# Performance work log

Measured on AMD Instinct MI355X. Metric: run time of the kernel, lower is better.

## Reference

```python
import jax, jax.numpy as jnp
import numpy as np

N, E, F_NODE, F_EDGE, HID, B, GDIM, ACT = 50000, 1600000, 32, 8, 256, 64, 16, 64
N_HIDDEN_LAYERS = 3


def setup_inputs() -> dict:
    key = jax.random.key(0)
    ks = jax.random.split(key, 16)
    x = jax.random.normal(ks[0], (N, F_NODE), jnp.float32)
    edge_index = jax.random.randint(ks[1], (2, E), 0, N, jnp.int64)
    edge_attr = jax.random.normal(ks[2], (E, F_EDGE), jnp.float32)
    batch = jnp.sort(jax.random.randint(ks[3], (N,), 0, B, jnp.int64))
    global_feats = jax.random.normal(ks[4], (B, GDIM), jnp.float32)
    s = lambda *d: 1.0 / np.sqrt(d[-2])
    # layer 0: node_feat -> hidden ; layers 1..3: hidden -> hidden
    We0 = jax.random.normal(ks[5], (F_EDGE, F_NODE), jnp.float32) * (1.0 / np.sqrt(F_EDGE))
    W0 = jax.random.normal(ks[6], (F_NODE, HID), jnp.float32) * (1.0 / np.sqrt(F_NODE))
    b0 = jnp.zeros((HID,), jnp.float32)
    We = jax.random.normal(ks[7], (N_HIDDEN_LAYERS, F_EDGE, HID), jnp.float32) * (1.0 / np.sqrt(F_EDGE))
    W = jax.random.normal(ks[8], (N_HIDDEN_LAYERS, HID, HID), jnp.float32) * (1.0 / np.sqrt(HID))
    b = jnp.zeros((N_HIDDEN_LAYERS, HID), jnp.float32)
    Wp = jax.random.normal(ks[9], (HID + GDIM, ACT), jnp.float32) * (1.0 / np.sqrt(HID + GDIM))
    bp = jnp.zeros((ACT,), jnp.float32)
    Wv = jax.random.normal(ks[10], (HID + GDIM, 1), jnp.float32) * (1.0 / np.sqrt(HID + GDIM))
    bv = jnp.zeros((1,), jnp.float32)
    return {"x": x, "edge_attr": edge_attr, "global_feats": global_feats,
            "We0": We0, "W0": W0, "b0": b0, "We": We, "W": W, "b": b,
            "Wp": Wp, "bp": bp, "Wv": Wv, "bv": bv,
            "edge_index": edge_index, "batch": batch}


def reference(x, edge_attr, global_feats, We0, W0, b0, We, W, b, Wp, bp, Wv, bv, edge_index, batch):
    src, dst = edge_index[0], edge_index[1]
    n_nodes = x.shape[0]
    n_graphs = global_feats.shape[0]

    def conv(h, We_l, W_l, b_l):
        # GINE-style: message relu(x_j + proj(e_ij)), sum-aggregate, node update MLP
        m = jax.nn.relu(h[src] + edge_attr @ We_l)            # [E, d]
        agg = jax.ops.segment_sum(m, dst, num_segments=n_nodes)
        return jax.nn.relu((h + agg) @ W_l + b_l)             # [N, hidden]

    h = conv(x, We0, W0, b0)
    for i in range(We.shape[0]):
        h = conv(h, We[i], W[i], b[i])

    counts = jax.ops.segment_sum(jnp.ones((n_nodes, 1), h.dtype), batch, num_segments=n_graphs)
    pooled = jax.ops.segment_sum(h, batch, num_segments=n_graphs) / jnp.maximum(counts, 1.0)
    feats = jnp.concatenate([pooled, global_feats], axis=-1)  # [B, hidden+gdim]
    logits = feats @ Wp + bp                                  # [B, max_action_dim]
    value = feats @ Wv + bv                                   # [B, 1]
    return logits, value
```

## Files before the change

kernel.cpp:

```cpp
#include <hip/hip_runtime.h>
#include <hip/hip_bf16.h>

#define NNODES 50000
#define NEDGES 1600000
#define FNODE 32
#define FEDGE 8
#define HIDD 256
#define NGRAPH 64
#define GDIM 16
#define NACT 64
#define FEATD (HIDD + GDIM)
#define PCH 8

typedef short bf16x8 __attribute__((ext_vector_type(8)));
typedef float f32x4 __attribute__((ext_vector_type(4)));
typedef __bf16 bf16x2 __attribute__((ext_vector_type(2)));


__device__ inline float bfl(uint u) {
  union { uint i; float f; } v; v.i = u << 16; return v.f;
}
__device__ inline float bfh(uint u) {
  union { uint i; float f; } v; v.i = u & 0xffff0000u; return v.f;
}
__device__ inline float bf1(ushort u) {
  union { uint i; float f; } v; v.i = ((uint)u) << 16; return v.f;
}
__device__ inline ushort f2b(float a) {
  __hip_bfloat16 h = __float2bfloat16(a);
  return *(ushort*)&h;
}
__device__ inline uint packbf(float a, float b) {
  return (uint)f2b(a) | ((uint)f2b(b) << 16);
}

__device__ inline float dot2bf(uint a, uint b, float c) {
#if defined(__has_builtin)
#if __has_builtin(__builtin_amdgcn_fdot2_f32_bf16)
  union { uint u; bf16x2 v; } ua, ub;
  ua.u = a; ub.u = b;
  return __builtin_amdgcn_fdot2_f32_bf16(ua.v, ub.v, c, false);
#else
  return fmaf(bfl(a), bfl(b), fmaf(bfh(a), bfh(b), c));
#endif
#else
  return fmaf(bfl(a), bfl(b), fmaf(bfh(a), bfh(b), c));
#endif
}


__global__ void k_zero_i32(int* __restrict__ p, int n) {
  int i = blockIdx.x * blockDim.x + threadIdx.x;
  if (i < n) p[i] = 0;
}

__global__ void k_scan1(int* __restrict__ data, int n, int* __restrict__ sums) {
  __shared__ int buf[1024];
  int gid = blockIdx.x * 1024 + threadIdx.x;
  int v = (gid < n) ? data[gid] : 0;
  buf[threadIdx.x] = v;
  __syncthreads();
  for (int d = 1; d < 1024; d <<= 1) {
    int t = (threadIdx.x >= d) ? buf[threadIdx.x - d] : 0;
    __syncthreads();
    buf[threadIdx.x] += t;
    __syncthreads();
  }
  if (gid < n) data[gid] = buf[threadIdx.x];
  if (threadIdx.x == 1023) sums[blockIdx.x] = buf[1023];
}

__global__ void k_scan3(int* __restrict__ data, int n, const int* __restrict__ sums,
                        int* __restrict__ cur) {
  int base = 0;
  for (int i = 0; i < (int)blockIdx.x; ++i) base += sums[i];
  int gid = blockIdx.x * 1024 + threadIdx.x;
  if (gid < n) {
    int v = data[gid] + base;
    data[gid] = v;
    if (gid < NNODES) cur[gid] = v;
  }
}

__global__ void k_scatter(const int* __restrict__ src, const int* __restrict__ dst,
                          int* __restrict__ cur, const float* __restrict__ ea,
                          int* __restrict__ csr_src, ushort* __restrict__ eab) {
  int e = blockIdx.x * blockDim.x + threadIdx.x;
  if (e >= NEDGES) return;
  int d = dst[e];
  int pos = atomicAdd(&cur[d], 1);
  csr_src[pos] = src[e] * 64;
  float4 a = *(const float4*)&ea[(size_t)e * FEDGE];
  float4 b = *(const float4*)&ea[(size_t)e * FEDGE + 4];
  uint4 o;
  o.x = packbf(a.x, a.y);
  o.y = packbf(a.z, a.w);
  o.z = packbf(b.x, b.y);
  o.w = packbf(b.z, b.w);
  *(uint4*)&eab[(size_t)pos * FEDGE] = o;
}


#define CVT_N (NNODES * FNODE / 4)
#define WEP_N (128 + 3 * 1024)
#define WP_N (1024 + 3 * 8192)

__global__ void k_hist_prep(const int* __restrict__ dst, int* __restrict__ off,
                            const float* __restrict__ x, ushort* __restrict__ xb,
                            const float* __restrict__ We0, const float* __restrict__ We,
                            uint* __restrict__ wep0, uint* __restrict__ wep,
                            const float* __restrict__ W0, const float* __restrict__ W,
                            ushort* __restrict__ wp0, ushort* __restrict__ wp) {
  int gid = blockIdx.x * blockDim.x + threadIdx.x;
  if (gid < NEDGES) atomicAdd(&off[dst[gid] + 1], 1);
  int i = gid;
  if (i < CVT_N) {
    float4 v = *(const float4*)&x[(size_t)i * 4];
    uint2 o;
    o.x = packbf(v.x, v.y);
    o.y = packbf(v.z, v.w);
    *(uint2*)&xb[(size_t)i * 4] = o;
    return;
  }
  i -= CVT_N;
  if (i < WEP_N) {
    if (i < 128) {
      int k2 = i >> 5, c = i & 31;
      wep0[i] = packbf(We0[(2 * k2) * FNODE + c], We0[(2 * k2 + 1) * FNODE + c]);
    } else {
      int u = i - 128;
      int l = u >> 10;
      int r = u & 1023;
      int k2 = r >> 8, c = r & 255;
      const float* Wl = We + (size_t)l * FEDGE * HIDD;
      wep[u] = packbf(Wl[(2 * k2) * HIDD + c], Wl[(2 * k2 + 1) * HIDD + c]);
    }
    return;
  }
  i -= WEP_N;
  if (i < WP_N) {
    if (i < 1024) {
      int lane = i & 63;
      int nf = i >> 6;
      int col = nf * 16 + (lane & 15);
      int k0 = (lane >> 4) * 8;
      ushort o[8];
#pragma unroll
      for (int q = 0; q < 8; ++q) o[q] = f2b(W0[(size_t)(k0 + q) * HIDD + col]);
      *(uint4*)&wp0[(size_t)i * 8] = *(uint4*)o;
    } else {
      int u = i - 1024;
      int l = u / 8192;
      int r = u - l * 8192;
      int lane = r & 63;
      int frag = r >> 6;
      int nf = frag & 15, ks = frag >> 4;
      int col = nf * 16 + (lane & 15);
      int k0 = ks * 32 + (lane >> 4) * 8;
      const float* Wl = W + (size_t)l * HIDD * HIDD;
      ushort o[8];
#pragma unroll
      for (int q = 0; q < 8; ++q) o[q] = f2b(Wl[(size_t)(k0 + q) * HIDD + col]);
      *(uint4*)&wp[(size_t)u * 8] = *(uint4*)o;
    }
  }
}


__global__ __launch_bounds__(256) void k_edge32(
    const float* __restrict__ x, const ushort* __restrict__ xb,
    const uint4* __restrict__ eab4, const uint* __restrict__ wep0,
    const int* __restrict__ off, const int* __restrict__ csr_src,
    ushort* __restrict__ t0b) {
  int wid = __builtin_amdgcn_readfirstlane(
      (int)((blockIdx.x * blockDim.x + threadIdx.x) >> 6));
  if (wid >= NNODES) return;
  int lane = threadIdx.x & 63;
  int j = lane >> 5;
  int c = lane & 31;
  uint c2 = (uint)c * 2;
  const char* xbase = (const char*)xb;
  uint w0 = wep0[c], w1 = wep0[32 + c], w2 = wep0[64 + c], w3 = wep0[96 + c];
  int s0 = off[wid], s1 = off[wid + 1];
  float acc = 0.f;
  int e = s0 + j;
  for (; e + 6 < s1; e += 8) {
    ushort hA = *(const ushort*)(xbase + ((uint)csr_src[e] + c2));
    ushort hB = *(const ushort*)(xbase + ((uint)csr_src[e + 2] + c2));
    ushort hC = *(const ushort*)(xbase + ((uint)csr_src[e + 4] + c2));
    ushort hD = *(const ushort*)(xbase + ((uint)csr_src[e + 6] + c2));
    uint4 eA = eab4[e];
    uint4 eB = eab4[e + 2];
    uint4 eC = eab4[e + 4];
    uint4 eD = eab4[e + 6];
    float pr;
#define B32(hu, eu)                 \
    pr = bf1(hu);                   \
    pr = dot2bf(eu.x, w0, pr);      \
    pr = dot2bf(eu.y, w1, pr);      \
    pr = dot2bf(eu.z, w2, pr);      \
    pr = dot2bf(eu.w, w3, pr);      \
    acc += fmaxf(pr, 0.f);
    B32(hA, eA) B32(hB, eB) B32(hC, eC) B32(hD, eD)
  }
  for (; e < s1; e += 2) {
    ushort hu = *(const ushort*)(xbase + ((uint)csr_src[e] + c2));
    uint4 eu = eab4[e];
    float pr;
    B32(hu, eu)
#undef B32
  }
  acc += __shfl_xor(acc, 32);
  if (j == 0) t0b[wid * FNODE + c] = f2b(x[wid * FNODE + c] + acc);
}


__device__ inline void body_dot(uint2 hu, uint4 eu, const uint4 wq[4], float4& acc) {
  float4 pr;
  pr.x = bfl(hu.x);
  pr.y = bfh(hu.x);
  pr.z = bfl(hu.y);
  pr.w = bfh(hu.y);
  pr.x = dot2bf(eu.x, wq[0].x, pr.x);
  pr.x = dot2bf(eu.y, wq[1].x, pr.x);
  pr.x = dot2bf(eu.z, wq[2].x, pr.x);
  pr.x = dot2bf(eu.w, wq[3].x, pr.x);
  pr.y = dot2bf(eu.x, wq[0].y, pr.y);
  pr.y = dot2bf(eu.y, wq[1].y, pr.y);
  pr.y = dot2bf(eu.z, wq[2].y, pr.y);
  pr.y = dot2bf(eu.w, wq[3].y, pr.y);
  pr.z = dot2bf(eu.x, wq[0].z, pr.z);
  pr.z = dot2bf(eu.y, wq[1].z, pr.z);
  pr.z = dot2bf(eu.z, wq[2].z, pr.z);
  pr.z = dot2bf(eu.w, wq[3].z, pr.z);
  pr.w = dot2bf(eu.x, wq[0].w, pr.w);
  pr.w = dot2bf(eu.y, wq[1].w, pr.w);
  pr.w = dot2bf(eu.z, wq[2].w, pr.w);
  pr.w = dot2bf(eu.w, wq[3].w, pr.w);
  acc.x += fmaxf(pr.x, 0.f);
  acc.y += fmaxf(pr.y, 0.f);
  acc.z += fmaxf(pr.z, 0.f);
  acc.w += fmaxf(pr.w, 0.f);
}

#define LOADCH(H, E_, eb)                                                   \
  _Pragma("unroll") for (int u = 0; u < 4; ++u) {                           \
    uint boff = ((uint)csr_src[(eb) + u] << 3) + c8;                        \
    H[u] = *(const uint2*)(hbase + boff);                                   \
  }                                                                         \
  _Pragma("unroll") for (int u = 0; u < 4; ++u) E_[u] = eab4[(eb) + u];

#define COMPCH(H, E_)                                                       \
  _Pragma("unroll") for (int u = 0; u < 4; ++u)                             \
    body_dot(H[u], E_[u], wq, (u & 1) ? acc1 : acc0);

__global__ __launch_bounds__(256) void k_edge256(
    const ushort* __restrict__ hb, const uint4* __restrict__ eab4,
    const uint* __restrict__ wepl, const int* __restrict__ off,
    const int* __restrict__ csr_src, ushort* __restrict__ tb) {
  int wid = __builtin_amdgcn_readfirstlane(
      (int)((blockIdx.x * blockDim.x + threadIdx.x) >> 6));
  if (wid >= NNODES) return;
  int lane = threadIdx.x & 63;
  int c = lane * 4;
  uint c8 = (uint)lane * 8;
  const char* hbase = (const char*)hb;
  uint4 wq[4];
#pragma unroll
  for (int k2 = 0; k2 < 4; ++k2) wq[k2] = *(const uint4*)&wepl[k2 * HIDD + c];
  int s0 = off[wid], s1 = off[wid + 1];
  float4 acc0 = {0.f, 0.f, 0.f, 0.f}, acc1 = {0.f, 0.f, 0.f, 0.f};
  int e = s0;
  int nch = (s1 - s0) >> 2;
  if (nch > 0) {
    uint2 hA[4], hB[4];
    uint4 EA[4], EB[4];
    LOADCH(hA, EA, e)
    int t = 1;
    for (; t + 1 < nch; t += 2) {
      LOADCH(hB, EB, e + 4)
      COMPCH(hA, EA)
      LOADCH(hA, EA, e + 8)
      COMPCH(hB, EB)
      e += 8;
    }
    if (t < nch) {
      LOADCH(hB, EB, e + 4)
      COMPCH(hA, EA)
      COMPCH(hB, EB)
      e += 8;
    } else {
      COMPCH(hA, EA)
      e += 4;
    }
  }
  for (; e < s1; ++e) {
    uint boff = ((uint)csr_src[e] << 3) + c8;
    uint2 hu = *(const uint2*)(hbase + boff);
    uint4 eu = eab4[e];
    body_dot(hu, eu, wq, acc0);
  }

  uint2 su = *(const uint2*)&hb[(size_t)wid * HIDD + c];
  float4 o;
  o.x = bfl(su.x) + acc0.x + acc1.x;
  o.y = bfh(su.x) + acc0.y + acc1.y;
  o.z = bfl(su.y) + acc0.z + acc1.z;
  o.w = bfh(su.y) + acc0.w + acc1.w;
  uint2 ob;
  ob.x = packbf(o.x, o.y);
  ob.y = packbf(o.z, o.w);
  *(uint2*)&tb[(size_t)wid * HIDD + c] = ob;
}
#undef LOADCH
#undef COMPCH


template <int K>
__global__ __launch_bounds__(256) void k_gemm_mfma(
    const ushort* __restrict__ Tb, const ushort* __restrict__ Wp,
    const float* __restrict__ bias, ushort* __restrict__ outb, int nrows) {
  constexpr int KS = K / 32;
  constexpr int KSH = (KS >= 2) ? 2 : KS;
  constexpr int CH = KSH * 16 * 64;
  __shared__ ushort bl[CH * 8];
  const int tid = threadIdx.x;
  const int wave = tid >> 6;
  const int lane = tid & 63;
  const int row0 = blockIdx.x * 64 + wave * 16;
  const int arow = row0 + (lane & 15);
  const int kgrp = lane >> 4;
  f32x4 acc[16];
#pragma unroll
  for (int nf = 0; nf < 16; ++nf) acc[nf] = (f32x4){0.f, 0.f, 0.f, 0.f};
#pragma unroll
  for (int st = 0; st < KS / KSH; ++st) {
    __syncthreads();
#pragma unroll
    for (int chk = 0; chk < CH / 256; ++chk) {
      int ch = chk * 256 + tid;
      *(uint4*)&bl[(size_t)ch * 8] = *(const uint4*)&Wp[((size_t)st * CH + ch) * 8];
    }
    __syncthreads();
#pragma unroll
    for (int ksl = 0; ksl < KSH; ++ksl) {
      int ks = st * KSH + ksl;
      bf16x8 af = *(const bf16x8*)&Tb[(size_t)arow * K + ks * 32 + kgrp * 8];
#pragma unroll
      for (int nf = 0; nf < 16; ++nf) {
        bf16x8 bfg = *(const bf16x8*)&bl[((size_t)(ksl * 16 + nf) * 64 + lane) * 8];
        acc[nf] = __builtin_amdgcn_mfma_f32_16x16x32_bf16(af, bfg, acc[nf], 0, 0, 0);
      }
    }
  }
  const int ocol0 = lane & 15;
  const int orow0 = row0 + (lane >> 4) * 4;
#pragma unroll
  for (int nf = 0; nf < 16; ++nf) {
    int col = nf * 16 + ocol0;
    float bv = bias[col];
#pragma unroll
    for (int r = 0; r < 4; ++r) {
      int row = orow0 + r;
      if (row < nrows) outb[(size_t)row * HIDD + col] = f2b(fmaxf(acc[nf][r] + bv, 0.f));
    }
  }
}


__global__ void k_pool_partial(const ushort* __restrict__ hb, const int* __restrict__ batch,
                               float* __restrict__ fp) {
  int b = blockIdx.x >> 3;
  int j = blockIdx.x & 7;
  __shared__ int srange[2];
  if (threadIdx.x < 2) {
    int target = b + threadIdx.x;
    int lo = 0, hi = NNODES;
    while (lo < hi) {
      int mid = (lo + hi) >> 1;
      if (batch[mid] < target) lo = mid + 1; else hi = mid;
    }
    srange[threadIdx.x] = lo;
  }
  __syncthreads();
  int s = srange[0], eend = srange[1];
  int len = eend - s;
  int cs = s + (int)((long long)len * j / PCH);
  int ce = s + (int)((long long)len * (j + 1) / PCH);
  int col = threadIdx.x;
  float acc = 0.f;
  for (int n = cs; n < ce; ++n) acc += bf1(hb[(size_t)n * HIDD + col]);
  fp[((size_t)j * NGRAPH + b) * HIDD + col] = acc;
}


__global__ void k_pool_heads(const float* __restrict__ fp, const int* __restrict__ batch,
                             const float* __restrict__ gf, const float* __restrict__ Wp,
                             const float* __restrict__ bp, const float* __restrict__ Wv,
                             const float* __restrict__ bv, float* __restrict__ out) {
  int b = blockIdx.x;
  __shared__ float f[FEATD];
  __shared__ int srange[2];
  if (threadIdx.x < 2) {
    int target = b + threadIdx.x;
    int lo = 0, hi = NNODES;
    while (lo < hi) {
      int mid = (lo + hi) >> 1;
      if (batch[mid] < target) lo = mid + 1; else hi = mid;
    }
    srange[threadIdx.x] = lo;
  }
  __syncthreads();
  int col = threadIdx.x;
  float acc = 0.f;
#pragma unroll
  for (int j = 0; j < PCH; ++j) acc += fp[((size_t)j * NGRAPH + b) * HIDD + col];
  float cnt = fmaxf((float)(srange[1] - srange[0]), 1.0f);
  f[col] = acc / cnt;
  if (col < GDIM) f[HIDD + col] = gf[b * GDIM + col];
  __syncthreads();
  if (col < NACT) {
    float lg = bp[col];
    for (int k = 0; k < FEATD; ++k) lg = fmaf(f[k], Wp[k * NACT + col], lg);
    out[b * NACT + col] = lg;
  } else if (col < 128) {
    int t = col - 64;
    float pv = 0.f;
    for (int k = t; k < FEATD; k += 64) pv = fmaf(f[k], Wv[k], pv);
#pragma unroll
    for (int d = 32; d > 0; d >>= 1) pv += __shfl_down(pv, d);
    if (t == 0) out[NGRAPH * NACT + b] = pv + bv[0];
  }
}


extern "C" void kernel_launch(void* const* d_in, const int* in_sizes, int n_in,
                              void* d_out, int out_size, void* d_ws, size_t ws_size,
                              hipStream_t stream) {
  const float* x   = (const float*)d_in[0];
  const float* ea  = (const float*)d_in[1];
  const float* gf  = (const float*)d_in[2];
  const float* We0 = (const float*)d_in[3];
  const float* W0  = (const float*)d_in[4];
  const float* b0  = (const float*)d_in[5];
  const float* We  = (const float*)d_in[6];
  const float* W   = (const float*)d_in[7];
  const float* bb  = (const float*)d_in[8];
  const float* Wp  = (const float*)d_in[9];
  const float* bp  = (const float*)d_in[10];
  const float* Wv  = (const float*)d_in[11];
  const float* bv  = (const float*)d_in[12];
  const int* eidx  = (const int*)d_in[13];
  const int* batch = (const int*)d_in[14];
  const int* esrc = eidx;
  const int* edst = eidx + NEDGES;

  char* w = (char*)d_ws;
  size_t p = 0;
  auto take = [&](size_t bytes) {
    size_t r = p;
    p += (bytes + 255) & ~(size_t)255;
    return r;
  };
  int* off      = (int*)(w + take((NNODES + 1) * 4));
  int* cur      = (int*)(w + take(NNODES * 4));
  int* sums     = (int*)(w + take(1024));
  int* csr_src  = (int*)(w + take((size_t)NEDGES * 4));
  ushort* eab   = (ushort*)(w + take((size_t)NEDGES * FEDGE * 2));
  ushort* t0b   = (ushort*)(w + take((size_t)NNODES * FNODE * 2));
  ushort* xb    = (ushort*)(w + take((size_t)NNODES * FNODE * 2));
  ushort* tb    = (ushort*)(w + take((size_t)NNODES * HIDD * 2));
  ushort* hb    = (ushort*)(w + take((size_t)NNODES * HIDD * 2));
  uint* wep0    = (uint*)(w + take(128 * 4));
  uint* wepb    = (uint*)(w + take(3 * 1024 * 4));
  ushort* wp0   = (ushort*)(w + take((size_t)1024 * 8 * 2));
  ushort* wpb   = (ushort*)(w + take((size_t)3 * 8192 * 8 * 2));
  float* fp     = (float*)(w + take((size_t)PCH * NGRAPH * HIDD * 4));
  if (p > ws_size) return;

  k_zero_i32<<<(NNODES + 1 + 255) / 256, 256, 0, stream>>>(off, NNODES + 1);
  k_hist_prep<<<(NEDGES + 255) / 256, 256, 0, stream>>>(
      edst, off, x, xb, We0, We, wep0, wepb, W0, W, wp0, wpb);
  int n_scan = NNODES + 1;
  int nb_scan = (n_scan + 1023) / 1024;
  k_scan1<<<nb_scan, 1024, 0, stream>>>(off, n_scan, sums);
  k_scan3<<<nb_scan, 1024, 0, stream>>>(off, n_scan, sums, cur);
  k_scatter<<<(NEDGES + 255) / 256, 256, 0, stream>>>(esrc, edst, cur, ea, csr_src, eab);

  const int gemm_grid = (NNODES + 63) / 64;

  k_edge32<<<NNODES / 4, 256, 0, stream>>>(x, xb, (const uint4*)eab, wep0, off,
                                           csr_src, t0b);
  k_gemm_mfma<FNODE><<<gemm_grid, 256, 0, stream>>>(t0b, wp0, b0, hb, NNODES);

  for (int l = 0; l < 3; ++l) {
    k_edge256<<<NNODES / 4, 256, 0, stream>>>(hb, (const uint4*)eab, wepb + l * 1024,
                                              off, csr_src, tb);
    k_gemm_mfma<HIDD><<<gemm_grid, 256, 0, stream>>>(
        tb, wpb + (size_t)l * 8192 * 8, bb + (size_t)l * HIDD, hb, NNODES);
  }

  k_pool_partial<<<NGRAPH * PCH, HIDD, 0, stream>>>(hb, batch, fp);
  k_pool_heads<<<NGRAPH, HIDD, 0, stream>>>(fp, batch, gf, Wp, bp, Wv, bv,
                                            (float*)d_out);
}
```

Baseline: 692.7 us.

## Split CSR scatter into permutation pass and gather-reorder; use fp32 FMA edge projection

The CSR build now scatters only edge ids through the atomic cursor, then a second kernel gathers src and edge attributes in destination order, so the writes to csr_src and eab become coalesced instead of random. This adds a kernel launch and an extra 1.6M-entry index array, and the gathers of src and edge_attr become random reads in exchange. Separately, the hidden-layer edge kernel unpacks the bf16 edge-projection weights to fp32 registers once and replaces the dot2 bf16 instructions with plain fp32 FMAs, which adds register pressure and per-edge unpack work for the edge features.

Measured after the change: 807.4 us. +16.6%, slower.

```diff
diff --git a/kernel.cpp b/kernel.cpp
--- a/kernel.cpp
+++ b/kernel.cpp
@@ -82,13 +82,20 @@
   }
 }
 
-__global__ void k_scatter(const int* __restrict__ src, const int* __restrict__ dst,
-                          int* __restrict__ cur, const float* __restrict__ ea,
-                          int* __restrict__ csr_src, ushort* __restrict__ eab) {
+__global__ void k_scatter_lite(const int* __restrict__ dst, int* __restrict__ cur,
+                               int* __restrict__ peid) {
   int e = blockIdx.x * blockDim.x + threadIdx.x;
   if (e >= NEDGES) return;
-  int d = dst[e];
-  int pos = atomicAdd(&cur[d], 1);
+  int pos = atomicAdd(&cur[dst[e]], 1);
+  peid[pos] = e;
+}
+
+__global__ void k_reorder(const int* __restrict__ peid, const int* __restrict__ src,
+                          const float* __restrict__ ea, int* __restrict__ csr_src,
+                          ushort* __restrict__ eab) {
+  int pos = blockIdx.x * blockDim.x + threadIdx.x;
+  if (pos >= NEDGES) return;
+  int e = peid[pos];
   csr_src[pos] = src[e] * 64;
   float4 a = *(const float4*)&ea[(size_t)e * FEDGE];
   float4 b = *(const float4*)&ea[(size_t)e * FEDGE + 4];
@@ -215,32 +222,22 @@
 }
 
 
-__device__ inline void body_dot(uint2 hu, uint4 eu, const uint4 wq[4], float4& acc) {
-  float4 pr;
-  pr.x = bfl(hu.x);
-  pr.y = bfh(hu.x);
-  pr.z = bfl(hu.y);
-  pr.w = bfh(hu.y);
-  pr.x = dot2bf(eu.x, wq[0].x, pr.x);
-  pr.x = dot2bf(eu.y, wq[1].x, pr.x);
-  pr.x = dot2bf(eu.z, wq[2].x, pr.x);
-  pr.x = dot2bf(eu.w, wq[3].x, pr.x);
-  pr.y = dot2bf(eu.x, wq[0].y, pr.y);
-  pr.y = dot2bf(eu.y, wq[1].y, pr.y);
-  pr.y = dot2bf(eu.z, wq[2].y, pr.y);
-  pr.y = dot2bf(eu.w, wq[3].y, pr.y);
-  pr.z = dot2bf(eu.x, wq[0].z, pr.z);
-  pr.z = dot2bf(eu.y, wq[1].z, pr.z);
-  pr.z = dot2bf(eu.z, wq[2].z, pr.z);
-  pr.z = dot2bf(eu.w, wq[3].z, pr.z);
-  pr.w = dot2bf(eu.x, wq[0].w, pr.w);
-  pr.w = dot2bf(eu.y, wq[1].w, pr.w);
-  pr.w = dot2bf(eu.z, wq[2].w, pr.w);
-  pr.w = dot2bf(eu.w, wq[3].w, pr.w);
-  acc.x += fmaxf(pr.x, 0.f);
-  acc.y += fmaxf(pr.y, 0.f);
-  acc.z += fmaxf(pr.z, 0.f);
-  acc.w += fmaxf(pr.w, 0.f);
+__device__ inline void body_f(uint2 hu, uint4 eu, const float wf[8][4], float4& acc) {
+  float ef0 = bfl(eu.x), ef1 = bfh(eu.x), ef2 = bfl(eu.y), ef3 = bfh(eu.y);
+  float ef4 = bfl(eu.z), ef5 = bfh(eu.z), ef6 = bfl(eu.w), ef7 = bfh(eu.w);
+  float p0 = bfl(hu.x), p1 = bfh(hu.x), p2 = bfl(hu.y), p3 = bfh(hu.y);
+#define FK(ef, k)                       \
+  p0 = fmaf(ef, wf[k][0], p0);          \
+  p1 = fmaf(ef, wf[k][1], p1);          \
+  p2 = fmaf(ef, wf[k][2], p2);          \
+  p3 = fmaf(ef, wf[k][3], p3);
+  FK(ef0, 0) FK(ef1, 1) FK(ef2, 2) FK(ef3, 3)
+  FK(ef4, 4) FK(ef5, 5) FK(ef6, 6) FK(ef7, 7)
+#undef FK
+  acc.x += fmaxf(p0, 0.f);
+  acc.y += fmaxf(p1, 0.f);
+  acc.z += fmaxf(p2, 0.f);
+  acc.w += fmaxf(p3, 0.f);
 }
 
 #define LOADCH(H, E_, eb)                                                   \
@@ -252,7 +249,7 @@
 
 #define COMPCH(H, E_)                                                       \
   _Pragma("unroll") for (int u = 0; u < 4; ++u)                             \
-    body_dot(H[u], E_[u], wq, (u & 1) ? acc1 : acc0);
+    body_f(H[u], E_[u], wf, (u & 1) ? acc1 : acc0);
 
 __global__ __launch_bounds__(256) void k_edge256(
     const ushort* __restrict__ hb, const uint4* __restrict__ eab4,
@@ -265,9 +262,15 @@
   int c = lane * 4;
   uint c8 = (uint)lane * 8;
   const char* hbase = (const char*)hb;
-  uint4 wq[4];
-#pragma unroll
-  for (int k2 = 0; k2 < 4; ++k2) wq[k2] = *(const uint4*)&wepl[k2 * HIDD + c];
+  float wf[8][4];
+#pragma unroll
+  for (int k2 = 0; k2 < 4; ++k2) {
+    uint4 pq = *(const uint4*)&wepl[k2 * HIDD + c];
+    wf[2 * k2][0] = bfl(pq.x); wf[2 * k2 + 1][0] = bfh(pq.x);
+    wf[2 * k2][1] = bfl(pq.y); wf[2 * k2 + 1][1] = bfh(pq.y);
+    wf[2 * k2][2] = bfl(pq.z); wf[2 * k2 + 1][2] = bfh(pq.z);
+    wf[2 * k2][3] = bfl(pq.w); wf[2 * k2 + 1][3] = bfh(pq.w);
+  }
   int s0 = off[wid], s1 = off[wid + 1];
   float4 acc0 = {0.f, 0.f, 0.f, 0.f}, acc1 = {0.f, 0.f, 0.f, 0.f};
   int e = s0;
@@ -298,7 +301,7 @@
     uint boff = ((uint)csr_src[e] << 3) + c8;
     uint2 hu = *(const uint2*)(hbase + boff);
     uint4 eu = eab4[e];
-    body_dot(hu, eu, wq, acc0);
+    body_f(hu, eu, wf, acc0);
   }
 
   uint2 su = *(const uint2*)&hb[(size_t)wid * HIDD + c];
@@ -465,6 +468,7 @@
   int* off      = (int*)(w + take((NNODES + 1) * 4));
   int* cur      = (int*)(w + take(NNODES * 4));
   int* sums     = (int*)(w + take(1024));
+  int* peid     = (int*)(w + take((size_t)NEDGES * 4));
   int* csr_src  = (int*)(w + take((size_t)NEDGES * 4));
   ushort* eab   = (ushort*)(w + take((size_t)NEDGES * FEDGE * 2));
   ushort* t0b   = (ushort*)(w + take((size_t)NNODES * FNODE * 2));
@@ -485,7 +489,8 @@
   int nb_scan = (n_scan + 1023) / 1024;
   k_scan1<<<nb_scan, 1024, 0, stream>>>(off, n_scan, sums);
   k_scan3<<<nb_scan, 1024, 0, stream>>>(off, n_scan, sums, cur);
-  k_scatter<<<(NEDGES + 255) / 256, 256, 0, stream>>>(esrc, edst, cur, ea, csr_src, eab);
+  k_scatter_lite<<<(NEDGES + 255) / 256, 256, 0, stream>>>(edst, cur, peid);
+  k_reorder<<<(NEDGES + 255) / 256, 256, 0, stream>>>(peid, esrc, ea, csr_src, eab);
 
   const int gemm_grid = (NNODES + 63) / 64;
 
```
